# Optimization experiments

Hardware: AMD Instinct MI355X
Metric: run time of the kernel (lower is better)

Reference implementation:

```python
import jax, jax.numpy as jnp
import numpy as np

EPS = 1e-8
MIN_VAL = -1e7  # module default min_val=-10000000.0


def _div_safe(n, d):
    return n / jnp.maximum(d, EPS)


def _cosine_pairwise(v1, v2):
    # v1: (B,L1,H), v2: (B,L2,H) -> (B,L1,L2)
    n1 = jnp.linalg.norm(v1, axis=2, keepdims=True)
    n2 = jnp.linalg.norm(v2, axis=2, keepdims=True)
    a = jnp.einsum('bik,bjk->bij', v1, v2)
    return _div_safe(a, n1 * jnp.swapaxes(n2, 1, 2))


def _masked_max(v, mask, axis, keepdims=False):
    rep = jnp.where(mask > 0, v, MIN_VAL)
    val = jnp.max(rep, axis=axis, keepdims=keepdims)
    m = jnp.max(jnp.broadcast_to(mask, v.shape), axis=axis, keepdims=keepdims)
    return val * m


def _masked_mean(v, mask, axis, keepdims=False):
    s = jnp.sum(v * mask, axis=axis, keepdims=keepdims)
    c = jnp.sum(jnp.broadcast_to(mask, v.shape), axis=axis, keepdims=keepdims)
    return _div_safe(s, c)


def _cos_sim(a, b, axis):
    # torch F.cosine_similarity semantics: dot / (max(|a|,eps)*max(|b|,eps))
    dot = jnp.sum(a * b, axis=axis)
    na = jnp.maximum(jnp.linalg.norm(a, axis=axis), EPS)
    nb = jnp.maximum(jnp.linalg.norm(b, axis=axis), EPS)
    return dot / (na * nb)


def _mpm(v1, v2, w):
    # v1, v2: (B,L,H); w: (P,H) -> ((B,L,1), (B,L,P))
    mv1 = _cos_sim(v1, v2, 2)[..., None]
    v1w = w[None, None] * v1[:, :, None, :]  # (B,L,P,H)
    v2w = w[None, None] * v2[:, :, None, :]
    return mv1, _cos_sim(v1w, v2w, 3)


def _mpm_pairwise(v1, v2, w):
    # v1: (B,L1,H), v2: (B,L2,H), w: (P,H) -> (B,L1,L2,P)
    v1w = w[None, :, None, :] * v1[:, None, :, :]  # (B,P,L1,H)
    v2w = w[None, :, None, :] * v2[:, None, :, :]  # (B,P,L2,H)
    n1 = jnp.linalg.norm(v1w, axis=3, keepdims=True)
    n2 = jnp.linalg.norm(v2w, axis=3, keepdims=True)
    n = jnp.einsum('bpik,bpjk->bpij', v1w, v2w)
    d = n1 * jnp.swapaxes(n2, 2, 3)
    return jnp.transpose(_div_safe(n, d), (0, 2, 3, 1))


def setup_inputs() -> dict:
    key = jax.random.key(0)
    ks = jax.random.split(key, 8)
    B, L, H, P = 32, 128, 100, 20
    return {
        'context_p': jax.random.normal(ks[0], (B, L, H), dtype=jnp.float32),
        'mask_p': jax.random.randint(ks[1], (B, L), 0, 2, dtype=jnp.int32),
        'context_h': jax.random.normal(ks[2], (B, L, H), dtype=jnp.float32),
        'mask_h': jax.random.randint(ks[3], (B, L), 0, 2, dtype=jnp.int32),
        'w0': jax.random.uniform(ks[4], (P, H), dtype=jnp.float32),
        'w1': jax.random.uniform(ks[5], (P, H), dtype=jnp.float32),
        'w2': jax.random.uniform(ks[6], (P, H), dtype=jnp.float32),
        'w3': jax.random.uniform(ks[7], (P, H), dtype=jnp.float32),
    }


def reference(context_p, mask_p, context_h, mask_h, w0, w1, w2, w3):
    mask_p = mask_p.astype(jnp.float32)
    mask_h = mask_h.astype(jnp.float32)
    B, Lp, H = context_p.shape
    Lh = context_h.shape[1]

    mask_p_h = mask_p[:, :, None] * mask_h[:, None, :]   # (B,Lp,Lh)
    mask_h_p = jnp.swapaxes(mask_p_h, 1, 2)              # (B,Lh,Lp)
    cp = context_p * mask_p[..., None]
    ch = context_h * mask_h[..., None]

    # --- pairwise cosine + masked max/mean pooling ---
    cos = _cosine_pairwise(cp, ch)                        # (B,Lp,Lh)
    cosT = jnp.swapaxes(cos, 1, 2)
    cos_max_p = _masked_max(cos, mask_p_h, 2, True)
    cos_mean_p = _masked_mean(cos, mask_p_h, 2, True)
    cos_max_h = _masked_max(cosT, mask_h_p, 2, True)
    cos_mean_h = _masked_mean(cosT, mask_h_p, 2, True)

    # --- full match (is_forward=True: last real token) ---
    idx_p = jnp.clip(jnp.sum(mask_p, 1).astype(jnp.int32) - 1, 0)[:, None, None]
    idx_h = jnp.clip(jnp.sum(mask_h, 1).astype(jnp.int32) - 1, 0)[:, None, None]
    cp_last = jnp.take_along_axis(cp, jnp.broadcast_to(idx_p, (B, 1, H)), axis=1)
    ch_last = jnp.take_along_axis(ch, jnp.broadcast_to(idx_h, (B, 1, H)), axis=1)
    mv_p_f1, mv_p_fP = _mpm(cp, jnp.broadcast_to(ch_last, (B, Lp, H)), w0)
    mv_h_f1, mv_h_fP = _mpm(ch, jnp.broadcast_to(cp_last, (B, Lh, H)), w0)

    # --- maxpool match ---
    mv_max = _mpm_pairwise(cp, ch, w1)                    # (B,Lp,Lh,P)
    mv_p_max = _masked_max(mv_max, mask_p_h[..., None], 2)
    mv_p_mean = _masked_mean(mv_max, mask_p_h[..., None], 2)
    mv_maxT = jnp.transpose(mv_max, (0, 2, 1, 3))
    mv_h_max = _masked_max(mv_maxT, mask_h_p[..., None], 2)
    mv_h_mean = _masked_mean(mv_maxT, mask_h_p[..., None], 2)

    # --- attentive match (mean) ---
    att_mean_h = _div_safe(jnp.einsum('bij,bjh->bih', cos, ch),
                           jnp.sum(cos, 2, keepdims=True))
    att_mean_p = _div_safe(jnp.einsum('bij,bih->bjh', cos, cp),
                           jnp.swapaxes(jnp.sum(cos, 1, keepdims=True), 1, 2))
    mv_p_am1, mv_p_amP = _mpm(cp, att_mean_h, w2)
    mv_h_am1, mv_h_amP = _mpm(ch, att_mean_p, w2)

    # --- max-attentive match ---
    att_h = ch[:, None, :, :] * cos[:, :, :, None]        # (B,Lp,Lh,H)
    att_p_t = cp[:, None, :, :] * cosT[:, :, :, None]     # (B,Lh,Lp,H) == att_p.permute(0,2,1,3)
    att_max_h = _masked_max(att_h, mask_p_h[..., None], 2)
    att_max_p = _masked_max(att_p_t, mask_h_p[..., None], 2)
    mv_p_ax1, mv_p_axP = _mpm(cp, att_max_h, w3)
    mv_h_ax1, mv_h_axP = _mpm(ch, att_max_p, w3)

    mv_p = jnp.concatenate([cos_max_p, cos_mean_p, mv_p_f1, mv_p_fP,
                            mv_p_max, mv_p_mean, mv_p_am1, mv_p_amP,
                            mv_p_ax1, mv_p_axP], axis=2)
    mv_h = jnp.concatenate([cos_max_h, cos_mean_h, mv_h_f1, mv_h_fP,
                            mv_h_max, mv_h_mean, mv_h_am1, mv_h_amP,
                            mv_h_ax1, mv_h_axP], axis=2)
    return mv_p, mv_h
```

## Files before the change

### kernel.cpp

```cpp
#include <hip/hip_runtime.h>
#include <math.h>


namespace {
constexpr int B = 32;
constexpr int L = 128;
constexpr int H = 100;
constexpr int P = 20;
constexpr int C = 105;
constexpr int TI = 8;
constexpr int SMEM_BYTES = 50176;
constexpr float EPSF = 1e-8f;
constexpr float MINV = -1e7f;
}

typedef unsigned short u16;
typedef unsigned int u32;
typedef short sh8 __attribute__((ext_vector_type(8)));
typedef float f4 __attribute__((ext_vector_type(4)));

__device__ __forceinline__ u16 f2bf(float f) {
    u32 u = __float_as_uint(f);
    u += 0x7FFFu + ((u >> 16) & 1u);
    return (u16)(u >> 16);
}
__device__ __forceinline__ float bf2f(u32 h) {
    return __uint_as_float(h << 16);
}

__global__ void k_prep(const float* __restrict__ ctx_p, const int* __restrict__ mask_p,
                       const float* __restrict__ ctx_h, const int* __restrict__ mask_h,
                       const float* __restrict__ w1,
                       float* __restrict__ cp, float* __restrict__ ch,
                       u16* __restrict__ cpb, u16* __restrict__ chb,
                       float* __restrict__ np_, float* __restrict__ nh_,
                       float* __restrict__ nwp, float* __restrict__ nwh)
{
    const int b = blockIdx.y, i = blockIdx.x, side = blockIdx.z, t = threadIdx.x;
    const float* ctx = side ? ctx_h : ctx_p;
    const int*  mask = side ? mask_h : mask_p;
    float* dst  = side ? ch  : cp;
    u16*   dstb = side ? chb : cpb;
    float* nrm  = side ? nh_ : np_;
    float* nw   = side ? nwh : nwp;

    const int row = b * L + i;
    __shared__ __align__(16) float sv2[H];
    const float m = (float)mask[row];
    float v = 0.f;
    if (t < H) {
        v = ctx[row * H + t] * m;
        dst[row * H + t] = v;
        sv2[t] = v * v;
    }
    dstb[row * 128 + t] = f2bf(v);
    __syncthreads();

    const int w = t >> 6, ln = t & 63;
    int g = -1, seg = 0;
    if (w == 0) { if (ln < 60) { g = ln / 5; seg = ln % 5; } }
    else        { if (ln < 45) { g = 12 + ln / 5; seg = ln % 5; } }
    if (g >= 0) {
        const float4* v4 = (const float4*)sv2;
        float acc = 0.f;
        if (g < P) {
            const float4* w4 = (const float4*)(w1 + g * H);
            #pragma unroll
            for (int k = seg * 5; k < seg * 5 + 5; ++k) {
                float4 wv_ = w4[k], s = v4[k];
                acc += wv_.x * wv_.x * s.x + wv_.y * wv_.y * s.y +
                       wv_.z * wv_.z * s.z + wv_.w * wv_.w * s.w;
            }
        } else {
            #pragma unroll
            for (int k = seg * 5; k < seg * 5 + 5; ++k) {
                float4 s = v4[k];
                acc += s.x + s.y + s.z + s.w;
            }
        }
        float a1 = __shfl(acc, ln + 1), a2 = __shfl(acc, ln + 2);
        float a3 = __shfl(acc, ln + 3), a4 = __shfl(acc, ln + 4);
        if (seg == 0) {
            float s = acc + a1 + a2 + a3 + a4;
            if (g < P) nw[row * P + g] = sqrtf(s);
            else       nrm[row] = sqrtf(s);
        }
    }
}

__global__ __launch_bounds__(256) void
k_main(const float* __restrict__ cp, const float* __restrict__ ch,
       const u16* __restrict__ cpb, const u16* __restrict__ chb,
       const float* __restrict__ np_, const float* __restrict__ nh_,
       const float* __restrict__ nw1p, const float* __restrict__ nw1h,
       const int* __restrict__ mask_p, const int* __restrict__ mask_h,
       const float* __restrict__ w0, const float* __restrict__ w1,
       const float* __restrict__ w2, const float* __restrict__ w3,
       float* __restrict__ out)
{
    __shared__ __align__(16) char smem[SMEM_BYTES];
    const int bx = blockIdx.x, b = blockIdx.y, t = threadIdx.x;
    const int wv = t >> 6, ln = t & 63;
    float* out_p = out;
    float* out_h = out + (size_t)B * L * C;

    if (bx < P) {
        const int p = bx;
        u16*  sB    = (u16*)smem;
        float* snwA = (float*)(smem + 34816);
        float* snwB = (float*)(smem + 35328);
        float* smA  = (float*)(smem + 35840);
        float* smB  = (float*)(smem + 36352);
        float* pJmax= (float*)(smem + 36864);
        float* pJsum= (float*)(smem + 37376);
        float* pImax= (float*)(smem + 37888);
        float* pIsum= (float*)(smem + 39936);
        float* sRed = (float*)(smem + 41984);

        if (t < 128) {
            snwA[t] = nw1p[(b * L + t) * P + p];
            snwB[t] = nw1h[(b * L + t) * P + p];
            smA[t] = (float)mask_p[b * L + t];
            smB[t] = (float)mask_h[b * L + t];
        }
        __syncthreads();

        if (t < 64) {
            float a0 = smB[t], a1 = smB[t + 64];
            float mx = fmaxf(a0, a1), sm = a0 + a1;
            for (int d = 1; d < 64; d <<= 1) {
                mx = fmaxf(mx, __shfl_xor(mx, d));
                sm += __shfl_xor(sm, d);
            }
            if (t == 0) { sRed[2] = mx; sRed[3] = sm; }
        } else if (t < 128) {
            const int l = t - 64;
            float a0 = smA[l], a1 = smA[l + 64];
            float mx = fmaxf(a0, a1), sm = a0 + a1;
            for (int d = 1; d < 64; d <<= 1) {
                mx = fmaxf(mx, __shfl_xor(mx, d));
                sm += __shfl_xor(sm, d);
            }
            if (l == 0) { sRed[0] = mx; sRed[1] = sm; }
        }

        {
            const uint4* src = (const uint4*)(chb + (size_t)b * L * 128);
            #pragma unroll
            for (int it = 0; it < 8; ++it) {
                int idx = it * 256 + t;
                int row = idx >> 4, kc = (idx & 15) * 8;
                uint4 v = src[idx];
                *(uint4*)&sB[row * 136 + kc] = v;
            }
        }
        __syncthreads();

        const int m = ln & 15, q = ln >> 4;

        float swv[4][8];
        #pragma unroll
        for (int ks = 0; ks < 4; ++ks)
            #pragma unroll
            for (int e = 0; e < 8; ++e) {
                int k = ks * 32 + q * 8 + e;
                float w = (k < H) ? w1[p * H + k] : 0.f;
                swv[ks][e] = w * w;
            }

        f4 acc[2][8];
        #pragma unroll
        for (int rt = 0; rt < 2; ++rt)
            #pragma unroll
            for (int ct = 0; ct < 8; ++ct)
                acc[rt][ct] = (f4){0.f, 0.f, 0.f, 0.f};

        const uint4* gA0 = (const uint4*)(cpb + (size_t)(b * L + wv * 32 + m) * 128);
        const uint4* gA1 = (const uint4*)(cpb + (size_t)(b * L + wv * 32 + 16 + m) * 128);

        #pragma unroll
        for (int ks = 0; ks < 4; ++ks) {
            uint4 va0 = gA0[ks * 4 + q];
            uint4 va1 = gA1[ks * 4 + q];
            sh8 a0, a1;
            {
                u32 vs0[4] = {va0.x, va0.y, va0.z, va0.w};
                u32 vs1[4] = {va1.x, va1.y, va1.z, va1.w};
                u32 r0[4], r1[4];
                #pragma unroll
                for (int e = 0; e < 4; ++e) {
                    float f0 = bf2f(vs0[e] & 0xffffu) * swv[ks][2 * e];
                    float f1 = bf2f(vs0[e] >> 16) * swv[ks][2 * e + 1];
                    r0[e] = (u32)f2bf(f0) | ((u32)f2bf(f1) << 16);
                    float g0 = bf2f(vs1[e] & 0xffffu) * swv[ks][2 * e];
                    float g1 = bf2f(vs1[e] >> 16) * swv[ks][2 * e + 1];
                    r1[e] = (u32)f2bf(g0) | ((u32)f2bf(g1) << 16);
                }
                uint4 o0 = {r0[0], r0[1], r0[2], r0[3]};
                uint4 o1 = {r1[0], r1[1], r1[2], r1[3]};
                a0 = __builtin_bit_cast(sh8, o0);
                a1 = __builtin_bit_cast(sh8, o1);
            }
            const int ko = ks * 32 + q * 8;
            #pragma unroll
            for (int ct = 0; ct < 8; ++ct) {
                sh8 bb = *(const sh8*)&sB[(ct * 16 + m) * 136 + ko];
                acc[0][ct] = __builtin_amdgcn_mfma_f32_16x16x32_bf16(a0, bb, acc[0][ct], 0, 0, 0);
                acc[1][ct] = __builtin_amdgcn_mfma_f32_16x16x32_bf16(a1, bb, acc[1][ct], 0, 0, 0);
            }
        }

        float nB[8], mBv[8], imax[8], isum[8];
        #pragma unroll
        for (int ct = 0; ct < 8; ++ct) {
            const int j = ct * 16 + m;
            nB[ct] = snwB[j]; mBv[ct] = smB[j];
            imax[ct] = MINV; isum[ct] = 0.f;
        }
        #pragma unroll
        for (int rt = 0; rt < 2; ++rt) {
            #pragma unroll
            for (int reg = 0; reg < 4; ++reg) {
                const int i = wv * 32 + rt * 16 + q * 4 + reg;
                const float na = snwA[i];
                const float ma = smA[i];
                float jmax = MINV, jsum = 0.f;
                #pragma unroll
                for (int ct = 0; ct < 8; ++ct) {
                    float v = acc[rt][ct][reg] *
                              __builtin_amdgcn_rcpf(fmaxf(na * nB[ct], EPSF));
                    jmax = fmaxf(jmax, mBv[ct] > 0.f ? v : MINV);
                    jsum += mBv[ct] > 0.f ? v : 0.f;
                    imax[ct] = fmaxf(imax[ct], ma > 0.f ? v : MINV);
                    isum[ct] += ma > 0.f ? v : 0.f;
                }
                for (int d = 1; d < 16; d <<= 1) {
                    jmax = fmaxf(jmax, __shfl_xor(jmax, d));
                    jsum += __shfl_xor(jsum, d);
                }
                if (m == 0) { pJmax[i] = jmax; pJsum[i] = jsum; }
            }
        }
        #pragma unroll
        for (int ct = 0; ct < 8; ++ct) {
            float mx = imax[ct], sm = isum[ct];
            mx = fmaxf(mx, __shfl_xor(mx, 16)); sm += __shfl_xor(sm, 16);
            mx = fmaxf(mx, __shfl_xor(mx, 32)); sm += __shfl_xor(sm, 32);
            if (q == 0) { const int j = ct * 16 + m; pImax[wv * 128 + j] = mx; pIsum[wv * 128 + j] = sm; }
        }
        __syncthreads();

        if (t < 128) {
            const int i = t;
            const float ma = smA[i];
            const float mm = ma * sRed[2];
            const float cnt = ma * sRed[3];
            float* orow = out_p + ((size_t)b * L + i) * C;
            orow[23 + p] = pJmax[i] * mm;
            orow[43 + p] = ma * pJsum[i] / fmaxf(cnt, EPSF);

            const float mb = smB[i];
            const float hmax = fmaxf(fmaxf(pImax[0 * 128 + i], pImax[1 * 128 + i]),
                                     fmaxf(pImax[2 * 128 + i], pImax[3 * 128 + i]));
            const float hsum = pIsum[0 * 128 + i] + pIsum[1 * 128 + i] +
                               pIsum[2 * 128 + i] + pIsum[3 * 128 + i];
            float* hrow = out_h + ((size_t)b * L + i) * C;
            hrow[23 + p] = hmax * mb * sRed[0];
            hrow[43 + p] = mb * hsum / fmaxf(mb * sRed[1], EPSF);
        }
    } else {
        const int e = bx - P;
        const int side = e >> 4, tile = e & 15;
        const int i0 = tile * TI;
        const float* A   = side ? ch : cp;
        const float* Bv  = side ? cp : ch;
        const u16*  Ab16 = side ? chb : cpb;
        const u16*  Bvb  = side ? cpb : chb;
        const float* nA_ = side ? nh_ : np_;
        const float* nB_ = side ? np_ : nh_;
        const int* maskA = side ? mask_h : mask_p;
        const int* maskB = side ? mask_p : mask_h;
        float* outBase = out + ((size_t)side * B * L + (size_t)b * L) * C;

        float* scosC = (float*)(smem + 34816);
        float* sa    = (float*)(smem + 38912);
        float* sam   = (float*)(smem + 42112);
        float* sax   = (float*)(smem + 45312);
        float* sl    = (float*)(smem + 48512);
        float* snB   = (float*)(smem + 48912);
        u16*  cidx  = (u16*)(smem + 49424);
        float* snA   = (float*)(smem + 49680);
        int*   pnv   = (int*)(smem + 49712);

        if (wv == 0) {
            int m0 = maskB[b * L + ln], m1 = maskB[b * L + 64 + ln];
            unsigned long long b0 = __ballot(m0 > 0);
            unsigned long long b1 = __ballot(m1 > 0);
            unsigned long long pre = (1ull << ln) - 1ull;
            int n0 = __popcll(b0);
            if (m0 > 0) cidx[__popcll(b0 & pre)] = (u16)ln;
            if (m1 > 0) cidx[n0 + __popcll(b1 & pre)] = (u16)(64 + ln);
            if (ln == 0) *pnv = n0 + __popcll(b1);
        } else if (wv >= 2) {
            for (int x = t - 128; x < TI * 128; x += 128) {
                int il = x >> 7, k = x & 127;
                if (k < H) sa[il * 100 + k] = A[((size_t)b * L + i0 + il) * H + k];
            }
        }
        __syncthreads();
        const int nv = *pnv;
        const int nct = (nv + 15) >> 4;

        {
            const uint4* src = (const uint4*)(Bvb + (size_t)b * L * 128);
            for (int c = t; c < nct * 256; c += 256) {
                int jj = c >> 4, cc = c & 15;
                uint4 v;
                if (jj < nv) v = src[(int)cidx[jj] * 16 + cc];
                else { v.x = v.y = v.z = v.w = 0u; }
                *(uint4*)(smem + jj * 272 + cc * 16) = v;
            }
            if (t < 128) snB[t] = (t < nv) ? nB_[b * L + (int)cidx[t]] : 0.f;
            else if (t < 136) snA[t - 128] = nA_[b * L + i0 + (t - 128)];
            if (wv == 1) {
                int last = nv - 1; if (last < 0) last = 0;
                const float* lr = Bv + ((size_t)b * L + last) * H;
                sl[ln] = lr[ln];
                if (ln + 64 < H) sl[ln + 64] = lr[ln + 64];
            }
        }
        __syncthreads();

        const int m = ln & 15, q = ln >> 4;
        {
            const uint4* gA = (const uint4*)(Ab16 + (size_t)(b * L + i0 + (m & 7)) * 128);
            f4 acc0 = (f4){0.f, 0.f, 0.f, 0.f};
            f4 acc1 = (f4){0.f, 0.f, 0.f, 0.f};
            const int ct0 = wv, ct1 = wv + 4;
            #pragma unroll
            for (int ks = 0; ks < 4; ++ks) {
                uint4 va = gA[ks * 4 + q];
                if (m >= 8) { va.x = va.y = va.z = va.w = 0u; }
                sh8 af = __builtin_bit_cast(sh8, va);
                const int ko2 = (ks * 32 + q * 8) * 2;
                if (ct0 < nct) {
                    sh8 bb = *(const sh8*)(smem + (ct0 * 16 + m) * 272 + ko2);
                    acc0 = __builtin_amdgcn_mfma_f32_16x16x32_bf16(af, bb, acc0, 0, 0, 0);
                }
                if (ct1 < nct) {
                    sh8 bb = *(const sh8*)(smem + (ct1 * 16 + m) * 272 + ko2);
                    acc1 = __builtin_amdgcn_mfma_f32_16x16x32_bf16(af, bb, acc1, 0, 0, 0);
                }
            }
            if (q < 2) {
                #pragma unroll
                for (int reg = 0; reg < 4; ++reg) {
                    const int i = q * 4 + reg;
                    const float ni = snA[i];
                    if (ct0 < nct) {
                        const int jj = ct0 * 16 + m;
                        scosC[i * 128 + jj] = acc0[reg] *
                            __builtin_amdgcn_rcpf(fmaxf(ni * snB[jj], EPSF));
                    }
                    if (ct1 < nct) {
                        const int jj = ct1 * 16 + m;
                        scosC[i * 128 + jj] = acc1[reg] *
                            __builtin_amdgcn_rcpf(fmaxf(ni * snB[jj], EPSF));
                    }
                }
            }
        }
        __syncthreads();

        #pragma unroll
        for (int pass = 0; pass < 2; ++pass) {
            const int il = wv + pass * 4;
            const int gi = i0 + il;
            if (ln < 50) {
                const float mA = (float)maskA[b * L + gi];
                float am0 = 0.f, am1 = 0.f, ax0 = MINV, ax1 = MINV;
                float scj = 0.f, cmx = MINV;
                const u32* bp = (const u32*)smem + ln;
                const float* cr = scosC + il * 128;
                #pragma unroll 4
                for (int jj = 0; jj < nv; ++jj) {
                    u32 pk = bp[jj * 68];
                    float cj = cr[jj];
                    scj += cj; cmx = fmaxf(cmx, cj);
                    float v0 = cj * __uint_as_float(pk << 16);
                    float v1 = cj * __uint_as_float(pk & 0xffff0000u);
                    am0 += v0; am1 += v1;
                    ax0 = fmaxf(ax0, v0); ax1 = fmaxf(ax1, v1);
                }
                const float rs = __builtin_amdgcn_rcpf(fmaxf(scj, EPSF));
                const float mm = (nv > 0) ? mA : 0.f;
                sam[il * 100 + 2 * ln] = am0 * rs; sam[il * 100 + 2 * ln + 1] = am1 * rs;
                sax[il * 100 + 2 * ln] = ax0 * mm; sax[il * 100 + 2 * ln + 1] = ax1 * mm;
                if (ln == 0) {
                    float* orow = outBase + (size_t)gi * C;
                    orow[0] = cmx * mm;
                    orow[1] = mA * scj / fmaxf(mA * (float)nv, EPSF);
                }
            }
        }
        __syncthreads();

        for (int task = t; task < TI * 63; task += 256) {
            const int il = task / 63, c = task - il * 63;
            float* orow = outBase + (size_t)(i0 + il) * C;
            const float4* a4 = (const float4*)(sa + il * 100);
            if (c < 60) {
                const int grp = c / 20, p = c - grp * 20;
                const float* wrow = (grp == 0 ? w0 : grp == 1 ? w2 : w3) + p * H;
                const float* oth = grp == 0 ? sl : (grp == 1 ? sam : sax) + il * 100;
                const float4* w4 = (const float4*)wrow;
                const float4* o4 = (const float4*)oth;
                float d = 0.f, na = 0.f, nb = 0.f;
                #pragma unroll 5
                for (int k = 0; k < H / 4; ++k) {
                    float4 w = w4[k], a = a4[k], o = o4[k];
                    float ww;
                    ww = w.x * w.x; d += ww * a.x * o.x; na += ww * a.x * a.x; nb += ww * o.x * o.x;
                    ww = w.y * w.y; d += ww * a.y * o.y; na += ww * a.y * a.y; nb += ww * o.y * o.y;
                    ww = w.z * w.z; d += ww * a.z * o.z; na += ww * a.z * a.z; nb += ww * o.z * o.z;
                    ww = w.w * w.w; d += ww * a.w * o.w; na += ww * a.w * a.w; nb += ww * o.w * o.w;
                }
                const int base = (grp == 0) ? 3 : (grp == 1) ? 64 : 85;
                orow[base + p] = d / (fmaxf(sqrtf(na), EPSF) * fmaxf(sqrtf(nb), EPSF));
            } else {
                const float* oth = (c == 60) ? sl : ((c == 61) ? sam : sax) + il * 100;
                const float4* o4 = (const float4*)oth;
                float d = 0.f, na = 0.f, nb = 0.f;
                #pragma unroll 5
                for (int k = 0; k < H / 4; ++k) {
                    float4 a = a4[k], o = o4[k];
                    d += a.x * o.x + a.y * o.y + a.z * o.z + a.w * o.w;
                    na += a.x * a.x + a.y * a.y + a.z * a.z + a.w * a.w;
                    nb += o.x * o.x + o.y * o.y + o.z * o.z + o.w * o.w;
                }
                orow[(c == 60) ? 2 : (c == 61) ? 63 : 84] =
                    d / (fmaxf(sqrtf(na), EPSF) * fmaxf(sqrtf(nb), EPSF));
            }
        }
    }
}

extern "C" void kernel_launch(void* const* d_in, const int* in_sizes, int n_in,
                              void* d_out, int out_size, void* d_ws, size_t ws_size,
                              hipStream_t stream)
{
    const float* ctx_p = (const float*)d_in[0];
    const int*   mask_p = (const int*)d_in[1];
    const float* ctx_h = (const float*)d_in[2];
    const int*   mask_h = (const int*)d_in[3];
    const float* w0 = (const float*)d_in[4];
    const float* w1 = (const float*)d_in[5];
    const float* w2 = (const float*)d_in[6];
    const float* w3 = (const float*)d_in[7];
    float* out = (float*)d_out;

    float* ws   = (float*)d_ws;
    float* cp   = ws;
    float* ch   = cp   + B * L * H;
    float* np_  = ch   + B * L * H;
    float* nh_  = np_  + B * L;
    float* nw1p = nh_  + B * L;
    float* nw1h = nw1p + B * L * P;
    u16*   cpb  = (u16*)(nw1h + B * L * P);
    u16*   chb  = cpb + B * L * 128;

    k_prep<<<dim3(L, B, 2), dim3(128), 0, stream>>>(
        ctx_p, mask_p, ctx_h, mask_h, w1,
        cp, ch, cpb, chb, np_, nh_, nw1p, nw1h);
    k_main<<<dim3(P + 32, B), dim3(256), 0, stream>>>(
        cp, ch, cpb, chb, np_, nh_, nw1p, nw1h, mask_p, mask_h,
        w0, w1, w2, w3, out);
}
```

Before: 136.7 us.

## Double k_main block size to 512 threads, halving per-wave work

Raises k_main to 512 threads (8 waves), giving each wave one 16-row MFMA tile instead of two in the pairwise-perspective blocks and one column tile in the attentive blocks. Shared-memory partial-reduction buffers are enlarged for eight waves, and the load and task loops use the new thread stride. The aim is more latency hiding and shorter per-wave serial chains, at the cost of fewer resident blocks per CU and more threads sitting idle in the small-work phases.

```diff
diff --git a/kernel.cpp b/kernel.cpp
--- a/kernel.cpp
+++ b/kernel.cpp
@@ -88,7 +88,7 @@
     }
 }
 
-__global__ __launch_bounds__(256) void
+__global__ __launch_bounds__(512) void
 k_main(const float* __restrict__ cp, const float* __restrict__ ch,
        const u16* __restrict__ cpb, const u16* __restrict__ chb,
        const float* __restrict__ np_, const float* __restrict__ nh_,
@@ -114,8 +114,8 @@
         float* pJmax= (float*)(smem + 36864);
         float* pJsum= (float*)(smem + 37376);
         float* pImax= (float*)(smem + 37888);
-        float* pIsum= (float*)(smem + 39936);
-        float* sRed = (float*)(smem + 41984);
+        float* pIsum= (float*)(smem + 41984);
+        float* sRed = (float*)(smem + 46080);
 
         if (t < 128) {
             snwA[t] = nw1p[(b * L + t) * P + p];
@@ -147,8 +147,8 @@
         {
             const uint4* src = (const uint4*)(chb + (size_t)b * L * 128);
             #pragma unroll
-            for (int it = 0; it < 8; ++it) {
-                int idx = it * 256 + t;
+            for (int it = 0; it < 4; ++it) {
+                int idx = it * 512 + t;
                 int row = idx >> 4, kc = (idx & 15) * 8;
                 uint4 v = src[idx];
                 *(uint4*)&sB[row * 136 + kc] = v;
@@ -168,45 +168,33 @@
                 swv[ks][e] = w * w;
             }
 
-        f4 acc[2][8];
-        #pragma unroll
-        for (int rt = 0; rt < 2; ++rt)
-            #pragma unroll
-            for (int ct = 0; ct < 8; ++ct)
-                acc[rt][ct] = (f4){0.f, 0.f, 0.f, 0.f};
-
-        const uint4* gA0 = (const uint4*)(cpb + (size_t)(b * L + wv * 32 + m) * 128);
-        const uint4* gA1 = (const uint4*)(cpb + (size_t)(b * L + wv * 32 + 16 + m) * 128);
+        f4 acc[8];
+        #pragma unroll
+        for (int ct = 0; ct < 8; ++ct) acc[ct] = (f4){0.f, 0.f, 0.f, 0.f};
+
+        const uint4* gA = (const uint4*)(cpb + (size_t)(b * L + wv * 16 + m) * 128);
 
         #pragma unroll
         for (int ks = 0; ks < 4; ++ks) {
-            uint4 va0 = gA0[ks * 4 + q];
-            uint4 va1 = gA1[ks * 4 + q];
-            sh8 a0, a1;
+            uint4 va = gA[ks * 4 + q];
+            sh8 af;
             {
-                u32 vs0[4] = {va0.x, va0.y, va0.z, va0.w};
-                u32 vs1[4] = {va1.x, va1.y, va1.z, va1.w};
-                u32 r0[4], r1[4];
+                u32 vs[4] = {va.x, va.y, va.z, va.w};
+                u32 r[4];
                 #pragma unroll
                 for (int e = 0; e < 4; ++e) {
-                    float f0 = bf2f(vs0[e] & 0xffffu) * swv[ks][2 * e];
-                    float f1 = bf2f(vs0[e] >> 16) * swv[ks][2 * e + 1];
-                    r0[e] = (u32)f2bf(f0) | ((u32)f2bf(f1) << 16);
-                    float g0 = bf2f(vs1[e] & 0xffffu) * swv[ks][2 * e];
-                    float g1 = bf2f(vs1[e] >> 16) * swv[ks][2 * e + 1];
-                    r1[e] = (u32)f2bf(g0) | ((u32)f2bf(g1) << 16);
-                }
-                uint4 o0 = {r0[0], r0[1], r0[2], r0[3]};
-                uint4 o1 = {r1[0], r1[1], r1[2], r1[3]};
-                a0 = __builtin_bit_cast(sh8, o0);
-                a1 = __builtin_bit_cast(sh8, o1);
+                    float f0 = bf2f(vs[e] & 0xffffu) * swv[ks][2 * e];
+                    float f1 = bf2f(vs[e] >> 16) * swv[ks][2 * e + 1];
+                    r[e] = (u32)f2bf(f0) | ((u32)f2bf(f1) << 16);
+                }
+                uint4 o = {r[0], r[1], r[2], r[3]};
+                af = __builtin_bit_cast(sh8, o);
             }
             const int ko = ks * 32 + q * 8;
             #pragma unroll
             for (int ct = 0; ct < 8; ++ct) {
                 sh8 bb = *(const sh8*)&sB[(ct * 16 + m) * 136 + ko];
-                acc[0][ct] = __builtin_amdgcn_mfma_f32_16x16x32_bf16(a0, bb, acc[0][ct], 0, 0, 0);
-                acc[1][ct] = __builtin_amdgcn_mfma_f32_16x16x32_bf16(a1, bb, acc[1][ct], 0, 0, 0);
+                acc[ct] = __builtin_amdgcn_mfma_f32_16x16x32_bf16(af, bb, acc[ct], 0, 0, 0);
             }
         }
 
@@ -218,28 +206,25 @@
             imax[ct] = MINV; isum[ct] = 0.f;
         }
         #pragma unroll
-        for (int rt = 0; rt < 2; ++rt) {
-            #pragma unroll
-            for (int reg = 0; reg < 4; ++reg) {
-                const int i = wv * 32 + rt * 16 + q * 4 + reg;
-                const float na = snwA[i];
-                const float ma = smA[i];
-                float jmax = MINV, jsum = 0.f;
-                #pragma unroll
-                for (int ct = 0; ct < 8; ++ct) {
-                    float v = acc[rt][ct][reg] *
-                              __builtin_amdgcn_rcpf(fmaxf(na * nB[ct], EPSF));
-                    jmax = fmaxf(jmax, mBv[ct] > 0.f ? v : MINV);
-                    jsum += mBv[ct] > 0.f ? v : 0.f;
-                    imax[ct] = fmaxf(imax[ct], ma > 0.f ? v : MINV);
-                    isum[ct] += ma > 0.f ? v : 0.f;
-                }
-                for (int d = 1; d < 16; d <<= 1) {
-                    jmax = fmaxf(jmax, __shfl_xor(jmax, d));
-                    jsum += __shfl_xor(jsum, d);
-                }
-                if (m == 0) { pJmax[i] = jmax; pJsum[i] = jsum; }
-            }
+        for (int reg = 0; reg < 4; ++reg) {
+            const int i = wv * 16 + q * 4 + reg;
+            const float na = snwA[i];
+            const float ma = smA[i];
+            float jmax = MINV, jsum = 0.f;
+            #pragma unroll
+            for (int ct = 0; ct < 8; ++ct) {
+                float v = acc[ct][reg] *
+                          __builtin_amdgcn_rcpf(fmaxf(na * nB[ct], EPSF));
+                jmax = fmaxf(jmax, mBv[ct] > 0.f ? v : MINV);
+                jsum += mBv[ct] > 0.f ? v : 0.f;
+                imax[ct] = fmaxf(imax[ct], ma > 0.f ? v : MINV);
+                isum[ct] += ma > 0.f ? v : 0.f;
+            }
+            for (int d = 1; d < 16; d <<= 1) {
+                jmax = fmaxf(jmax, __shfl_xor(jmax, d));
+                jsum += __shfl_xor(jsum, d);
+            }
+            if (m == 0) { pJmax[i] = jmax; pJsum[i] = jsum; }
         }
         #pragma unroll
         for (int ct = 0; ct < 8; ++ct) {
@@ -260,10 +245,12 @@
             orow[43 + p] = ma * pJsum[i] / fmaxf(cnt, EPSF);
 
             const float mb = smB[i];
-            const float hmax = fmaxf(fmaxf(pImax[0 * 128 + i], pImax[1 * 128 + i]),
-                                     fmaxf(pImax[2 * 128 + i], pImax[3 * 128 + i]));
-            const float hsum = pIsum[0 * 128 + i] + pIsum[1 * 128 + i] +
-                               pIsum[2 * 128 + i] + pIsum[3 * 128 + i];
+            float hmax = MINV, hsum = 0.f;
+            #pragma unroll
+            for (int s = 0; s < 8; ++s) {
+                hmax = fmaxf(hmax, pImax[s * 128 + i]);
+                hsum += pIsum[s * 128 + i];
+            }
             float* hrow = out_h + ((size_t)b * L + i) * C;
             hrow[23 + p] = hmax * mb * sRed[0];
             hrow[43 + p] = mb * hsum / fmaxf(mb * sRed[1], EPSF);
@@ -302,7 +289,7 @@
             if (m1 > 0) cidx[n0 + __popcll(b1 & pre)] = (u16)(64 + ln);
             if (ln == 0) *pnv = n0 + __popcll(b1);
         } else if (wv >= 2) {
-            for (int x = t - 128; x < TI * 128; x += 128) {
+            for (int x = t - 128; x < TI * 128; x += 384) {
                 int il = x >> 7, k = x & 127;
                 if (k < H) sa[il * 100 + k] = A[((size_t)b * L + i0 + il) * H + k];
             }
@@ -313,7 +300,7 @@
 
         {
             const uint4* src = (const uint4*)(Bvb + (size_t)b * L * 128);
-            for (int c = t; c < nct * 256; c += 256) {
+            for (int c = t; c < nct * 256; c += 512) {
                 int jj = c >> 4, cc = c & 15;
                 uint4 v;
                 if (jj < nv) v = src[(int)cidx[jj] * 16 + cc];
@@ -332,49 +319,32 @@
         __syncthreads();
 
         const int m = ln & 15, q = ln >> 4;
-        {
+        if (wv < nct) {
             const uint4* gA = (const uint4*)(Ab16 + (size_t)(b * L + i0 + (m & 7)) * 128);
             f4 acc0 = (f4){0.f, 0.f, 0.f, 0.f};
-            f4 acc1 = (f4){0.f, 0.f, 0.f, 0.f};
-            const int ct0 = wv, ct1 = wv + 4;
             #pragma unroll
             for (int ks = 0; ks < 4; ++ks) {
                 uint4 va = gA[ks * 4 + q];
                 if (m >= 8) { va.x = va.y = va.z = va.w = 0u; }
                 sh8 af = __builtin_bit_cast(sh8, va);
                 const int ko2 = (ks * 32 + q * 8) * 2;
-                if (ct0 < nct) {
-                    sh8 bb = *(const sh8*)(smem + (ct0 * 16 + m) * 272 + ko2);
-                    acc0 = __builtin_amdgcn_mfma_f32_16x16x32_bf16(af, bb, acc0, 0, 0, 0);
-                }
-                if (ct1 < nct) {
-                    sh8 bb = *(const sh8*)(smem + (ct1 * 16 + m) * 272 + ko2);
-                    acc1 = __builtin_amdgcn_mfma_f32_16x16x32_bf16(af, bb, acc1, 0, 0, 0);
-                }
+                sh8 bb = *(const sh8*)(smem + (wv * 16 + m) * 272 + ko2);
+                acc0 = __builtin_amdgcn_mfma_f32_16x16x32_bf16(af, bb, acc0, 0, 0, 0);
             }
             if (q < 2) {
                 #pragma unroll
                 for (int reg = 0; reg < 4; ++reg) {
                     const int i = q * 4 + reg;
-                    const float ni = snA[i];
-                    if (ct0 < nct) {
-                        const int jj = ct0 * 16 + m;
-                        scosC[i * 128 + jj] = acc0[reg] *
-                            __builtin_amdgcn_rcpf(fmaxf(ni * snB[jj], EPSF));
-                    }
-                    if (ct1 < nct) {
-                        const int jj = ct1 * 16 + m;
-                        scosC[i * 128 + jj] = acc1[reg] *
-                            __builtin_amdgcn_rcpf(fmaxf(ni * snB[jj], EPSF));
-                    }
-                }
-            }
-        }
-        __syncthreads();
-
-        #pragma unroll
-        for (int pass = 0; pass < 2; ++pass) {
-            const int il = wv + pass * 4;
+                    const int jj = wv * 16 + m;
+                    scosC[i * 128 + jj] = acc0[reg] *
+                        __builtin_amdgcn_rcpf(fmaxf(snA[i] * snB[jj], EPSF));
+                }
+            }
+        }
+        __syncthreads();
+
+        {
+            const int il = wv;
             const int gi = i0 + il;
             if (ln < 50) {
                 const float mA = (float)maskA[b * L + gi];
@@ -405,7 +375,7 @@
         }
         __syncthreads();
 
-        for (int task = t; task < TI * 63; task += 256) {
+        for (int task = t; task < TI * 63; task += 512) {
             const int il = task / 63, c = task - il * 63;
             float* orow = outBase + (size_t)(i0 + il) * C;
             const float4* a4 = (const float4*)(sa + il * 100);
@@ -472,7 +442,7 @@
     k_prep<<<dim3(L, B, 2), dim3(128), 0, stream>>>(
         ctx_p, mask_p, ctx_h, mask_h, w1,
         cp, ch, cpb, chb, np_, nh_, nw1p, nw1h);
-    k_main<<<dim3(P + 32, B), dim3(256), 0, stream>>>(
+    k_main<<<dim3(P + 32, B), dim3(512), 0, stream>>>(
         cp, ch, cpb, chb, np_, nh_, nw1p, nw1h, mask_p, mask_h,
         w0, w1, w2, w3, out);
 }
```

Measured after the change: 124.7 us. 1.1x faster.
